# Kernel tuning notes

Hardware: AMD Instinct MI355X
Metric: run time of the kernel (lower is better)

Reference implementation:

```python
import jax, jax.numpy as jnp
import numpy as np

ALPHA = 0.05  # init kwarg `alpha`


def _image_gradients(img):
    """tf.image.image_gradients semantics: returns (dy, dx), each same shape as
    img, with the last row (dy) / last column (dx) zero-padded."""
    dy = jnp.concatenate([img[:, 1:, :, :] - img[:, :-1, :, :],
                          jnp.zeros_like(img[:, :1, :, :])], axis=1)
    dx = jnp.concatenate([img[:, :, 1:, :] - img[:, :, :-1, :],
                          jnp.zeros_like(img[:, :, :1, :])], axis=2)
    return dy, dx


def _bilinear_warp(img, flow):
    """Backward-warp img by flow: sample img at (x + u, y + v), bilinear,
    coordinates clamped to the image border."""
    B, H, W, C = img.shape
    gy = jnp.arange(H, dtype=img.dtype)[:, None]  # [H,1]
    gx = jnp.arange(W, dtype=img.dtype)[None, :]  # [1,W]
    x = jnp.clip(gx + flow[..., 0], 0.0, W - 1)   # [B,H,W]
    y = jnp.clip(gy + flow[..., 1], 0.0, H - 1)
    x0f = jnp.floor(x)
    y0f = jnp.floor(y)
    x0 = x0f.astype(jnp.int32)
    y0 = y0f.astype(jnp.int32)
    x1 = jnp.minimum(x0 + 1, W - 1)
    y1 = jnp.minimum(y0 + 1, H - 1)
    wx = (x - x0f)[..., None]  # [B,H,W,1]
    wy = (y - y0f)[..., None]

    flat = img.reshape(B, H * W, C)

    def gather(yi, xi):
        idx = (yi * W + xi).reshape(B, H * W, 1)
        return jnp.take_along_axis(flat, idx, axis=1).reshape(B, H, W, C)

    Ia = gather(y0, x0)
    Ib = gather(y0, x1)
    Ic = gather(y1, x0)
    Id = gather(y1, x1)
    return (Ia * (1 - wx) + Ib * wx) * (1 - wy) + (Ic * (1 - wx) + Id * wx) * wy


def setup_inputs() -> dict:
    key = jax.random.key(0)
    k1, k2, k3 = jax.random.split(key, 3)
    B, H, W = 32, 512, 512
    I1 = jax.random.normal(k1, (B, H, W, 1), dtype=jnp.float32)
    I2 = jax.random.normal(k2, (B, H, W, 1), dtype=jnp.float32)
    flow = jax.random.normal(k3, (B, H, W, 2), dtype=jnp.float32)
    return {"I1": I1, "I2": I2, "flow": flow}


def reference(I1, I2, flow):
    # NOTE: tf.image.image_gradients returns (dy, dx); the original code unpacks
    # the first return into `grad_x`, so we faithfully reproduce that swap.
    I1_grad_x, I1_grad_y = _image_gradients(I1)  # actually (dy, dx) per TF
    # I2 gradients are computed but unused in the original forward.
    I2_warped = _bilinear_warp(I2, flow)
    u = flow[:, :, :, 0]
    v = flow[:, :, :, 1]
    dataTerm = I2_warped - I1
    u_next = u - ALPHA * dataTerm[:, :, :, 0] * I1_grad_x[:, :, :, 0]
    v_next = v - ALPHA * dataTerm[:, :, :, 0] * I1_grad_y[:, :, :, 0]
    return jnp.stack([u_next, v_next], axis=-1)
```

## Files before the change

### kernel.cpp

```cpp
#include <hip/hip_runtime.h>

#define ALPHA 0.05f

typedef float f32x4 __attribute__((ext_vector_type(4)));
typedef float f32x2 __attribute__((ext_vector_type(2)));

constexpr int RW = 84, RH = 49;
constexpr int CH4 = RW / 4;
constexpr int LDS_N = RW * RH;

__global__ __launch_bounds__(256) void dataterm_kernel(
    const float* __restrict__ I1,
    const float* __restrict__ I2,
    const float* __restrict__ flow,
    float* __restrict__ out)
{
    __shared__ float s_i2[LDS_N];

    int blk = blockIdx.x;
    int tx0 = (blk & 7) << 6;
    int ty0 = ((blk >> 3) & 15) << 5;
    int b   = blk >> 7;
    int base = b << 18;

    const float* I2b = I2 + base;
    const float* I1b = I1 + base;
    int tid = threadIdx.x;

    if (tx0 >= 64 && tx0 <= 384) {
        const float* src = I2b + tx0 - 8;
        for (int i = tid; i < CH4 * RH; i += 256) {
            int r  = i / CH4;
            int c4 = (i - r * CH4) << 2;
            int sy = min(max(ty0 - 8 + r, 0), 511);
            *reinterpret_cast<f32x4*>(&s_i2[r * RW + c4]) =
                *reinterpret_cast<const f32x4*>(src + (sy << 9) + c4);
        }
    } else {
        for (int i = tid; i < LDS_N; i += 256) {
            int r = i / RW;
            int c = i - r * RW;
            int sy = min(max(ty0 - 8 + r, 0), 511);
            int sx = min(max(tx0 - 8 + c, 0), 511);
            s_i2[i] = I2b[(sy << 9) + sx];
        }
    }
    __syncthreads();

    int lx = tid & 31;
    int g  = tid >> 5;
    int x  = tx0 + (lx << 1);

#pragma unroll
    for (int j = 0; j < 4; ++j) {
        int y   = ty0 + g + (j << 3);
        int pix = (y << 9) + x;

        f32x4 fA = __builtin_nontemporal_load(
            reinterpret_cast<const f32x4*>(flow + 2 * (base + pix)));
        f32x2 i1v = *reinterpret_cast<const f32x2*>(I1b + pix);
        float i1n = (x < 510) ? I1b[pix + 2] : 0.0f;
        f32x2 i1d = (y < 511) ? *reinterpret_cast<const f32x2*>(I1b + pix + 512)
                              : i1v;

        float i1a[2]  = { i1v.x, i1v.y };
        float i1ra[2] = { i1v.y, i1n  };
        float i1ba[2] = { i1d.x, i1d.y };
        float ua[2]   = { fA.x, fA.z };
        float va[2]   = { fA.y, fA.w };
        float un[2], vn[2];

#pragma unroll
        for (int k = 0; k < 2; ++k) {
            int xk = x + k;
            float u = ua[k], v = va[k];
            float g_dy = i1ba[k] - i1a[k];
            float g_dx = (xk < 511) ? (i1ra[k] - i1a[k]) : 0.0f;

            float xx = fminf(fmaxf((float)xk + u, 0.0f), 511.0f);
            float yy = fminf(fmaxf((float)y  + v, 0.0f), 511.0f);
            float x0f = floorf(xx);
            float y0f = floorf(yy);
            int x0 = (int)x0f;
            int y0 = (int)y0f;
            float wx = xx - x0f;
            float wy = yy - y0f;

            float Ia, Ib_, Ic, Id;
            bool oob = fmaxf(fabsf(u), fabsf(v)) > 8.0f;
            if (__builtin_expect(!oob, 1)) {
                int lidx = (y0 - ty0 + 8) * RW + (x0 - tx0 + 8);
                Ia  = s_i2[lidx];
                Ib_ = s_i2[lidx + 1];
                Ic  = s_i2[lidx + RW];
                Id  = s_i2[lidx + RW + 1];
            } else {
                int x1 = min(x0 + 1, 511);
                int y1 = min(y0 + 1, 511);
                Ia  = I2b[(y0 << 9) + x0];
                Ib_ = I2b[(y0 << 9) + x1];
                Ic  = I2b[(y1 << 9) + x0];
                Id  = I2b[(y1 << 9) + x1];
            }

            float top = Ia + wx * (Ib_ - Ia);
            float bot = Ic + wx * (Id - Ic);
            float warped = top + wy * (bot - top);

            float dt = warped - i1a[k];
            un[k] = u - ALPHA * dt * g_dy;
            vn[k] = v - ALPHA * dt * g_dx;
        }

        f32x4 ov;
        ov.x = un[0]; ov.y = vn[0]; ov.z = un[1]; ov.w = vn[1];
        __builtin_nontemporal_store(ov,
            reinterpret_cast<f32x4*>(out + 2 * (base + pix)));
    }
}

extern "C" void kernel_launch(void* const* d_in, const int* in_sizes, int n_in,
                              void* d_out, int out_size, void* d_ws, size_t ws_size,
                              hipStream_t stream) {
    const float* I1   = (const float*)d_in[0];
    const float* I2   = (const float*)d_in[1];
    const float* flow = (const float*)d_in[2];
    float* out = (float*)d_out;

    dataterm_kernel<<<4096, 256, 0, stream>>>(I1, I2, flow, out);
}
```

Measured before the change: 43.47 us.

## Stage I2 halo via direct global-to-LDS loads and prefetch per-thread operands early

The I2 halo tile is now filled with 16-byte global_load_lds transfers that write straight into LDS instead of passing through registers, using one uniform clamped path in place of the separate vector and scalar edge paths. Each thread now handles four consecutive rows instead of rows strided by eight. Its flow and I1 loads are issued before the barrier so they overlap the halo fetch, and I1 rows are reused between neighbouring rows for the vertical gradient. This trades higher register pressure and a slightly larger LDS allocation for fewer global I1 reads and better latency hiding.

Result: no change. 43.32 us (-0.4%).

```diff
diff --git a/kernel.cpp b/kernel.cpp
--- a/kernel.cpp
+++ b/kernel.cpp
@@ -6,8 +6,9 @@
 typedef float f32x2 __attribute__((ext_vector_type(2)));
 
 constexpr int RW = 84, RH = 49;
-constexpr int CH4 = RW / 4;
-constexpr int LDS_N = RW * RH;
+constexpr int CH = 21;
+constexpr int NCHUNK = CH * RH;
+constexpr int LDS_FLOATS = 5 * 256 * 4;
 
 __global__ __launch_bounds__(256) void dataterm_kernel(
     const float* __restrict__ I1,
@@ -15,7 +16,7 @@
     const float* __restrict__ flow,
     float* __restrict__ out)
 {
-    __shared__ float s_i2[LDS_N];
+    __shared__ float s_i2[LDS_FLOATS];
 
     int blk = blockIdx.x;
     int tx0 = (blk & 7) << 6;
@@ -27,47 +28,56 @@
     const float* I1b = I1 + base;
     int tid = threadIdx.x;
 
-    if (tx0 >= 64 && tx0 <= 384) {
-        const float* src = I2b + tx0 - 8;
-        for (int i = tid; i < CH4 * RH; i += 256) {
-            int r  = i / CH4;
-            int c4 = (i - r * CH4) << 2;
-            int sy = min(max(ty0 - 8 + r, 0), 511);
-            *reinterpret_cast<f32x4*>(&s_i2[r * RW + c4]) =
-                *reinterpret_cast<const f32x4*>(src + (sy << 9) + c4);
-        }
-    } else {
-        for (int i = tid; i < LDS_N; i += 256) {
-            int r = i / RW;
-            int c = i - r * RW;
-            int sy = min(max(ty0 - 8 + r, 0), 511);
-            int sx = min(max(tx0 - 8 + c, 0), 511);
-            s_i2[i] = I2b[(sy << 9) + sx];
-        }
+    int lx = tid & 31;
+    int rg = tid >> 5;
+    int x  = tx0 + (lx << 1);
+    int yb = ty0 + (rg << 2);
+    int pix0 = (yb << 9) + x;
+
+    f32x4 fA[4];
+    f32x2 rowv[5];
+    float i1n[4];
+#pragma unroll
+    for (int j = 0; j < 4; ++j)
+        fA[j] = __builtin_nontemporal_load(
+            reinterpret_cast<const f32x4*>(flow + 2 * (base + pix0 + (j << 9))));
+#pragma unroll
+    for (int j = 0; j < 4; ++j)
+        rowv[j] = *reinterpret_cast<const f32x2*>(I1b + pix0 + (j << 9));
+    rowv[4] = (yb + 4 < 512)
+        ? *reinterpret_cast<const f32x2*>(I1b + pix0 + (4 << 9)) : rowv[3];
+#pragma unroll
+    for (int j = 0; j < 4; ++j)
+        i1n[j] = (x < 510) ? I1b[pix0 + (j << 9) + 2] : 0.0f;
+
+    int wave = tid >> 6;
+    int lane = tid & 63;
+#pragma unroll
+    for (int p = 0; p < 5; ++p) {
+        int cb = (p << 8) + (wave << 6);
+        int i  = cb + lane;
+        int r  = i / 21;
+        int c4 = (i - r * 21) << 2;
+        int sy = min(max(ty0 - 8 + r, 0), 511);
+        int gx = min(max(tx0 - 8 + c4, 0), 508);
+        const float* g = I2b + (sy << 9) + gx;
+        __builtin_amdgcn_global_load_lds(
+            (const __attribute__((address_space(1))) void*)g,
+            (__attribute__((address_space(3))) void*)(s_i2 + (cb << 2)),
+            16, 0, 0);
     }
     __syncthreads();
 
-    int lx = tid & 31;
-    int g  = tid >> 5;
-    int x  = tx0 + (lx << 1);
-
 #pragma unroll
     for (int j = 0; j < 4; ++j) {
-        int y   = ty0 + g + (j << 3);
-        int pix = (y << 9) + x;
+        int y   = yb + j;
+        int pix = pix0 + (j << 9);
 
-        f32x4 fA = __builtin_nontemporal_load(
-            reinterpret_cast<const f32x4*>(flow + 2 * (base + pix)));
-        f32x2 i1v = *reinterpret_cast<const f32x2*>(I1b + pix);
-        float i1n = (x < 510) ? I1b[pix + 2] : 0.0f;
-        f32x2 i1d = (y < 511) ? *reinterpret_cast<const f32x2*>(I1b + pix + 512)
-                              : i1v;
-
-        float i1a[2]  = { i1v.x, i1v.y };
-        float i1ra[2] = { i1v.y, i1n  };
-        float i1ba[2] = { i1d.x, i1d.y };
-        float ua[2]   = { fA.x, fA.z };
-        float va[2]   = { fA.y, fA.w };
+        float ua[2] = { fA[j].x, fA[j].z };
+        float va[2] = { fA[j].y, fA[j].w };
+        float i1a[2]  = { rowv[j].x, rowv[j].y };
+        float i1ra[2] = { rowv[j].y, i1n[j] };
+        float i1ba[2] = { rowv[j + 1].x, rowv[j + 1].y };
         float un[2], vn[2];
 
 #pragma unroll
```
